# Optimization experiments

Hardware: AMD Instinct MI355X
Metric: run time of the kernel (lower is better)

## Reference

```python
import jax, jax.numpy as jnp
import numpy as np

SIGMA = 8.0       # init: sigma
BG_RATIO = 0.15   # init: background_ratio
C_SIZE = 512      # init: c_size
STRIDE = 8        # init: stride
B, N = 32, 512    # images, points per image (ragged regularized to fixed N)


def setup_inputs() -> dict:
    key = jax.random.key(0)
    k1, k2 = jax.random.split(key)
    # head coordinates uniform over the crop, in pixels
    points = jax.random.uniform(k1, (B, N, 2), dtype=jnp.float32) * C_SIZE
    # shortest-side sizes per image, in [256, 512]
    st_sizes = 256.0 + jax.random.uniform(k2, (B,), dtype=jnp.float32) * 256.0
    # grid-cell center coordinates, as built in __init__
    cood = jnp.arange(0, C_SIZE, STRIDE, dtype=jnp.float32) + STRIDE / 2  # [C]
    return {"points": points, "st_sizes": st_sizes, "cood": cood}


def _post_prob_one(pts, st_size, cood):
    # pts: [N, 2], st_size: scalar, cood: [C]
    x = pts[:, 0:1]                      # [N, 1]
    y = pts[:, 1:2]                      # [N, 1]
    c = cood[None, :]                    # [1, C]
    x_dis = x * x - 2.0 * x * c + c * c  # [N, C] squared dist along x
    y_dis = y * y - 2.0 * y * c + c * c  # [N, C] squared dist along y
    n = pts.shape[0]
    # dis[n, i, j] = y_dis[n, i] + x_dis[n, j], flattened to [N, C*C]
    dis = (y_dis[:, :, None] + x_dis[:, None, :]).reshape(n, -1)
    # background term: squared distance from each pixel to its nearest point
    min_dis = jnp.clip(jnp.min(dis, axis=0, keepdims=True), 0.0)  # [1, C*C]
    d = st_size * BG_RATIO
    bg_dis = (d - jnp.sqrt(min_dis)) ** 2                          # [1, C*C]
    full = jnp.concatenate([dis, bg_dis], axis=0)                  # [N+1, C*C]
    # softmax over points (+ background) for each pixel
    return jax.nn.softmax(-full / (2.0 * SIGMA ** 2), axis=0)


def reference(points, st_sizes, cood):
    # vmap over images replaces the per-image Python loop of the original
    return jax.vmap(lambda p, s: _post_prob_one(p, s, cood))(points, st_sizes)  # [B, N+1, C*C]
```

## Files before the change

### kernel.cpp

```cpp
#include <hip/hip_runtime.h>

#define NPTS 512
#define KINV (-0.0078125f)

typedef float v4f __attribute__((ext_vector_type(4)));

__global__ __launch_bounds__(256) void k_denom(
    const float* __restrict__ pts,
    const float* __restrict__ st,
    const float* __restrict__ cood,
    float* __restrict__ out,
    float* __restrict__ rinv)
{
    __shared__ __align__(16) float2 s_p[NPTS];
    __shared__ float s_sum[4][64];
    __shared__ float s_min[4][64];

    const int b   = blockIdx.x >> 6;
    const int i   = blockIdx.x & 63;
    const int tid = threadIdx.x;
    const float ci = cood[i];

    for (int t = tid; t < NPTS; t += 256) {
        float2 p = ((const float2*)pts)[b * NPTS + t];
        float yd = p.y - ci;
        s_p[t] = make_float2(p.x, yd * yd);
    }
    __syncthreads();

    const int j = tid & 63;
    const int q = tid >> 6;
    const float cj = cood[j];
    float sum0 = 0.0f, sum1 = 0.0f;
    float mn0 = 3.4e38f, mn1 = 3.4e38f;
    const v4f* sp4 = (const v4f*)s_p;
    const int t0 = q * 64;
    #pragma unroll 8
    for (int t = t0; t < t0 + 64; ++t) {
        v4f v = sp4[t];
        float xd0 = v.x - cj;
        float a0  = fmaf(xd0, xd0, v.y);
        float xd1 = v.z - cj;
        float a1  = fmaf(xd1, xd1, v.w);
        sum0 += __expf(a0 * KINV);
        sum1 += __expf(a1 * KINV);
        mn0 = fminf(mn0, a0);
        mn1 = fminf(mn1, a1);
    }
    s_sum[q][j] = sum0 + sum1;
    s_min[q][j] = fminf(mn0, mn1);
    __syncthreads();

    if (tid < 64) {
        float S = (s_sum[0][tid] + s_sum[1][tid]) + (s_sum[2][tid] + s_sum[3][tid]);
        float m = fminf(fminf(s_min[0][tid], s_min[1][tid]),
                        fminf(s_min[2][tid], s_min[3][tid]));
        m = fmaxf(m, 0.0f);
        float dd = st[b] * 0.15f;
        float bd = dd - sqrtf(m);
        float bg = __expf(bd * bd * KINV);
        S += bg;
        float r = 1.0f / S;
        rinv[b * 4096 + i * 64 + tid] = r;
        out[(size_t)(b * 513 + 512) * 4096 + i * 64 + tid] = bg * r;
    }
}

#define RSTRIDE 17

__global__ __launch_bounds__(256) void k_write(
    const float* __restrict__ pts,
    const float* __restrict__ cood,
    const float* __restrict__ rinv,
    float* __restrict__ out)
{
    __shared__ __align__(16) float s_rinv[64 * RSTRIDE * 4];
    __shared__ __align__(16) float s_ex[16 * 64];
    __shared__ float s_ey[16 * 64];

    const int b   = blockIdx.x >> 5;
    const int n0  = (blockIdx.x & 31) * 16;
    const int tid = threadIdx.x;

    const float4* rsrc = (const float4*)(rinv + b * 4096);
    float4* rdst = (float4*)s_rinv;
    for (int t = tid; t < 1024; t += 256) {
        int row = t >> 4, col = t & 15;
        rdst[row * RSTRIDE + col] = rsrc[t];
    }

    for (int t = tid; t < 1024; t += 256) {
        int nl = t >> 6;
        int jj = t & 63;
        float2 p = ((const float2*)pts)[b * NPTS + n0 + nl];
        float c  = cood[jj];
        float xd = p.x - c;
        float yd = p.y - c;
        s_ex[t] = __expf(xd * xd * KINV);
        s_ey[t] = __expf(yd * yd * KINV);
    }
    __syncthreads();

    v4f* dst = (v4f*)(out + (size_t)(b * 513 + n0) * 4096);
    const v4f* sx4 = (const v4f*)s_ex;
    const v4f* sr4 = (const v4f*)s_rinv;
    #pragma unroll 4
    for (int it = 0; it < 64; ++it) {
        int idx = it * 256 + tid;
        int nl  = idx >> 10;
        int c4  = idx & 1023;
        int ii  = c4 >> 4;
        int j4  = c4 & 15;
        v4f ex4 = sx4[nl * 16 + j4];
        v4f r4  = sr4[ii * RSTRIDE + j4];
        float ey = s_ey[nl * 64 + ii];
        v4f o = ey * ex4 * r4;
        __builtin_nontemporal_store(o, &dst[idx]);
    }
}

extern "C" void kernel_launch(void* const* d_in, const int* in_sizes, int n_in,
                              void* d_out, int out_size, void* d_ws, size_t ws_size,
                              hipStream_t stream) {
    const float* pts  = (const float*)d_in[0];
    const float* st   = (const float*)d_in[1];
    const float* cood = (const float*)d_in[2];
    float* out  = (float*)d_out;
    float* rinv = (float*)d_ws;

    k_denom<<<dim3(2048), dim3(256), 0, stream>>>(pts, st, cood, out, rinv);
    k_write<<<dim3(1024), dim3(256), 0, stream>>>(pts, cood, rinv, out);
}
```

Baseline: 286.2 us.

## Process two grid rows per denom block and hoist rinv loads in writer

k_denom now handles two y-rows per block, loading raw points once with a single float4 per thread and computing y distances inline, which halves the grid and reuses x distances across both rows. k_write keeps four rinv vectors in registers per thread and loops over points instead of recomputing indices, cutting shared-memory reads. The writer also switches from nontemporal stores to ordinary stores, which may change cache behaviour for the large output write.

Measured after the change: 275.0 us. 3.9% less time.

```diff
diff --git a/kernel.cpp b/kernel.cpp
--- a/kernel.cpp
+++ b/kernel.cpp
@@ -12,57 +12,62 @@
     float* __restrict__ out,
     float* __restrict__ rinv)
 {
-    __shared__ __align__(16) float2 s_p[NPTS];
-    __shared__ float s_sum[4][64];
-    __shared__ float s_min[4][64];
+    __shared__ __align__(16) float s_p[NPTS * 2];
+    __shared__ float s_sum[4][2][64];
+    __shared__ float s_min[4][2][64];
 
-    const int b   = blockIdx.x >> 6;
-    const int i   = blockIdx.x & 63;
+    const int b   = blockIdx.x >> 5;
+    const int i0  = (blockIdx.x & 31) * 2;
     const int tid = threadIdx.x;
-    const float ci = cood[i];
+    const float ci0 = cood[i0];
+    const float ci1 = cood[i0 + 1];
 
-    for (int t = tid; t < NPTS; t += 256) {
-        float2 p = ((const float2*)pts)[b * NPTS + t];
-        float yd = p.y - ci;
-        s_p[t] = make_float2(p.x, yd * yd);
-    }
+    ((float4*)s_p)[tid] = ((const float4*)(pts + b * (NPTS * 2)))[tid];
     __syncthreads();
 
     const int j = tid & 63;
     const int q = tid >> 6;
     const float cj = cood[j];
-    float sum0 = 0.0f, sum1 = 0.0f;
-    float mn0 = 3.4e38f, mn1 = 3.4e38f;
+    float sA0 = 0.0f, sA1 = 0.0f, sB0 = 0.0f, sB1 = 0.0f;
+    float m00 = 3.4e38f, m01 = 3.4e38f, m10 = 3.4e38f, m11 = 3.4e38f;
     const v4f* sp4 = (const v4f*)s_p;
     const int t0 = q * 64;
     #pragma unroll 8
     for (int t = t0; t < t0 + 64; ++t) {
         v4f v = sp4[t];
-        float xd0 = v.x - cj;
-        float a0  = fmaf(xd0, xd0, v.y);
-        float xd1 = v.z - cj;
-        float a1  = fmaf(xd1, xd1, v.w);
-        sum0 += __expf(a0 * KINV);
-        sum1 += __expf(a1 * KINV);
-        mn0 = fminf(mn0, a0);
-        mn1 = fminf(mn1, a1);
+        float xd0 = v.x - cj; float x20 = xd0 * xd0;
+        float xd1 = v.z - cj; float x21 = xd1 * xd1;
+        float ya = v.y - ci0; float a00 = fmaf(ya, ya, x20);
+        float yb = v.y - ci1; float a01 = fmaf(yb, yb, x20);
+        float yc = v.w - ci0; float a10 = fmaf(yc, yc, x21);
+        float yd = v.w - ci1; float a11 = fmaf(yd, yd, x21);
+        sA0 += __expf(a00 * KINV);  sB0 += __expf(a10 * KINV);
+        sA1 += __expf(a01 * KINV);  sB1 += __expf(a11 * KINV);
+        m00 = fminf(m00, a00);  m10 = fminf(m10, a10);
+        m01 = fminf(m01, a01);  m11 = fminf(m11, a11);
     }
-    s_sum[q][j] = sum0 + sum1;
-    s_min[q][j] = fminf(mn0, mn1);
+    s_sum[q][0][j] = sA0 + sB0;
+    s_sum[q][1][j] = sA1 + sB1;
+    s_min[q][0][j] = fminf(m00, m10);
+    s_min[q][1][j] = fminf(m01, m11);
     __syncthreads();
 
-    if (tid < 64) {
-        float S = (s_sum[0][tid] + s_sum[1][tid]) + (s_sum[2][tid] + s_sum[3][tid]);
-        float m = fminf(fminf(s_min[0][tid], s_min[1][tid]),
-                        fminf(s_min[2][tid], s_min[3][tid]));
+    if (tid < 128) {
+        int ii = tid >> 6;
+        int c  = tid & 63;
+        float S = (s_sum[0][ii][c] + s_sum[1][ii][c]) +
+                  (s_sum[2][ii][c] + s_sum[3][ii][c]);
+        float m = fminf(fminf(s_min[0][ii][c], s_min[1][ii][c]),
+                        fminf(s_min[2][ii][c], s_min[3][ii][c]));
         m = fmaxf(m, 0.0f);
         float dd = st[b] * 0.15f;
         float bd = dd - sqrtf(m);
         float bg = __expf(bd * bd * KINV);
         S += bg;
         float r = 1.0f / S;
-        rinv[b * 4096 + i * 64 + tid] = r;
-        out[(size_t)(b * 513 + 512) * 4096 + i * 64 + tid] = bg * r;
+        int ig = i0 + ii;
+        rinv[b * 4096 + ig * 64 + c] = r;
+        out[(size_t)(b * 513 + 512) * 4096 + ig * 64 + c] = bg * r;
     }
 }
 
@@ -101,21 +106,28 @@
     }
     __syncthreads();
 
+    const int j4     = tid & 15;
+    const int iibase = tid >> 4;
+    const v4f* sr4 = (const v4f*)s_rinv;
+    const v4f* sx4 = (const v4f*)s_ex;
+    v4f r0 = sr4[(iibase +  0) * RSTRIDE + j4];
+    v4f r1 = sr4[(iibase + 16) * RSTRIDE + j4];
+    v4f r2 = sr4[(iibase + 32) * RSTRIDE + j4];
+    v4f r3 = sr4[(iibase + 48) * RSTRIDE + j4];
+
     v4f* dst = (v4f*)(out + (size_t)(b * 513 + n0) * 4096);
-    const v4f* sx4 = (const v4f*)s_ex;
-    const v4f* sr4 = (const v4f*)s_rinv;
     #pragma unroll 4
-    for (int it = 0; it < 64; ++it) {
-        int idx = it * 256 + tid;
-        int nl  = idx >> 10;
-        int c4  = idx & 1023;
-        int ii  = c4 >> 4;
-        int j4  = c4 & 15;
+    for (int nl = 0; nl < 16; ++nl) {
         v4f ex4 = sx4[nl * 16 + j4];
-        v4f r4  = sr4[ii * RSTRIDE + j4];
-        float ey = s_ey[nl * 64 + ii];
-        v4f o = ey * ex4 * r4;
-        __builtin_nontemporal_store(o, &dst[idx]);
+        float ey0 = s_ey[nl * 64 + iibase +  0];
+        float ey1 = s_ey[nl * 64 + iibase + 16];
+        float ey2 = s_ey[nl * 64 + iibase + 32];
+        float ey3 = s_ey[nl * 64 + iibase + 48];
+        int base = nl * 1024 + tid;
+        dst[base +   0] = (ey0 * ex4) * r0;
+        dst[base + 256] = (ey1 * ex4) * r1;
+        dst[base + 512] = (ey2 * ex4) * r2;
+        dst[base + 768] = (ey3 * ex4) * r3;
     }
 }
 
@@ -128,6 +140,6 @@
     float* out  = (float*)d_out;
     float* rinv = (float*)d_ws;
 
-    k_denom<<<dim3(2048), dim3(256), 0, stream>>>(pts, st, cood, out, rinv);
+    k_denom<<<dim3(1024), dim3(256), 0, stream>>>(pts, st, cood, out, rinv);
     k_write<<<dim3(1024), dim3(256), 0, stream>>>(pts, cood, rinv, out);
 }
```
